# Optimization experiments

Hardware: AMD Instinct MI355X
Metric: run time of the kernel (lower is better)

## Reference

```python
import jax, jax.numpy as jnp
import numpy as np

# Graph sampling geometry (2-layer neighbor sampling, fanouts 16 and 10)
N0 = 1_048_576   # layer-0 src nodes (full frontier, features supplied)
N1 = 65_536      # layer-0 dst nodes == layer-1 src nodes
N2 = 4_096       # layer-1 dst nodes (seeds)
DEG0, DEG1 = 16, 10
E0, E1 = N1 * DEG0, N2 * DEG1
D_IN, D_H, D_OUT = 128, 256, 47


def _init_linear(key, out_f, in_f):
    s = 1.0 / np.sqrt(in_f)
    return jax.random.uniform(key, (out_f, in_f), jnp.float32, -s, s)


def setup_inputs() -> dict:
    key = jax.random.key(0)
    ks = jax.random.split(key, 10)
    x = jax.random.normal(ks[0], (N0, D_IN), dtype=jnp.float32)
    # CSC: indptr over dst nodes (uniform degree), indices = src node ids
    indptr0 = jnp.arange(N1 + 1, dtype=jnp.int32) * DEG0
    indices0 = jax.random.randint(ks[1], (E0,), 0, N0, dtype=jnp.int32)
    indptr1 = jnp.arange(N2 + 1, dtype=jnp.int32) * DEG1
    indices1 = jax.random.randint(ks[2], (E1,), 0, N1, dtype=jnp.int32)
    return {
        "x": x,
        "indices0": indices0, "indptr0": indptr0,
        "indices1": indices1, "indptr1": indptr1,
        "Wl0": _init_linear(ks[3], D_H, D_IN), "bl0": jnp.zeros((D_H,), jnp.float32),
        "Wr0": _init_linear(ks[4], D_H, D_IN),
        "Wl1": _init_linear(ks[5], D_H, D_H), "bl1": jnp.zeros((D_H,), jnp.float32),
        "Wr1": _init_linear(ks[6], D_H, D_H),
        "Wo": _init_linear(ks[7], D_OUT, D_H), "bo": jnp.zeros((D_OUT,), jnp.float32),
    }


def expand_indptr(indptr, num_edges):
    # gb.expand_indptr: edge e -> dst j with indptr[j] <= e < indptr[j+1]
    e = jnp.arange(num_edges, dtype=indptr.dtype)
    return jnp.searchsorted(indptr, e, side="right") - 1


def sage_conv(h, src, dst, dst_size, Wl, bl, Wr):
    # PyG SAGEConv (mean aggr): lin_l(mean_{neighbors}) + lin_r(x_dst)
    msg = h[src]                                                    # [E, d]
    summed = jax.ops.segment_sum(msg, dst, num_segments=dst_size)  # [dst, d]
    cnt = jax.ops.segment_sum(jnp.ones_like(dst, dtype=h.dtype), dst,
                              num_segments=dst_size)
    mean = summed / jnp.maximum(cnt, 1.0)[:, None]
    return mean @ Wl.T + bl + h[:dst_size] @ Wr.T


def reference(x, indices0, indptr0, indices1, indptr1,
              Wl0, bl0, Wr0, Wl1, bl1, Wr1, Wo, bo):
    # layer 0
    dst0 = expand_indptr(indptr0, E0)
    h = sage_conv(x, indices0, dst0, N1, Wl0, bl0, Wr0)
    h = jax.nn.gelu(h, approximate=False)  # dropout p=0.0 -> identity
    # layer 1
    dst1 = expand_indptr(indptr1, E1)
    h = sage_conv(h, indices1, dst1, N2, Wl1, bl1, Wr1)
    h = jax.nn.gelu(h, approximate=False)
    # final projection
    return h @ Wo.T + bo
```

## Files before the change

### kernel.cpp

```cpp
#include <hip/hip_runtime.h>
#include <math.h>

#define N0 1048576
#define N1 65536
#define N2 4096
#define DEG0 16
#define DEG1 10
#define D_IN 128
#define D_H 256
#define D_OUT 47

typedef unsigned int uint32;
typedef __attribute__((ext_vector_type(8))) short bf16x8;
typedef __attribute__((ext_vector_type(4))) float f32x4;

__device__ __forceinline__ unsigned short f2b(float x) {
    uint32 u = __float_as_uint(x);
    return (unsigned short)((u + 0x7fffu + ((u >> 16) & 1u)) >> 16);
}
__device__ __forceinline__ float b2f(unsigned short h) {
    return __uint_as_float(((uint32)h) << 16);
}
__device__ __forceinline__ float gelu_exact(float x) {
    return 0.5f * x * (1.0f + erff(x * 0.70710678118654752f));
}
__device__ __forceinline__ void split4(const float4 v, ushort4& h, ushort4& l) {
    h.x = f2b(v.x); l.x = f2b(v.x - b2f(h.x));
    h.y = f2b(v.y); l.y = f2b(v.y - b2f(h.y));
    h.z = f2b(v.z); l.z = f2b(v.z - b2f(h.z));
    h.w = f2b(v.w); l.w = f2b(v.w - b2f(h.w));
}

__global__ __launch_bounds__(256) void prep_all(
    const float4* __restrict__ Wl0, const float4* __restrict__ Wr0,
    const float4* __restrict__ Wl1, const float4* __restrict__ Wr1,
    const float4* __restrict__ Wo,  const float* __restrict__ bo,
    ushort4* __restrict__ wl0h, ushort4* __restrict__ wl0l,
    ushort4* __restrict__ wr0h, ushort4* __restrict__ wr0l,
    ushort4* __restrict__ wl1h, ushort4* __restrict__ wl1l,
    ushort4* __restrict__ wr1h, ushort4* __restrict__ wr1l,
    ushort4* __restrict__ woh,  ushort4* __restrict__ wol,
    float* __restrict__ bo_pad)
{
    int i = blockIdx.x * 256 + threadIdx.x;
    if (i >= 53248) return;
    const float4* src; ushort4 *dh, *dl; int rel;
    if (i < 8192)       { rel = i;         src = Wl0 + rel; dh = wl0h + rel; dl = wl0l + rel; }
    else if (i < 16384) { rel = i - 8192;  src = Wr0 + rel; dh = wr0h + rel; dl = wr0l + rel; }
    else if (i < 32768) { rel = i - 16384; src = Wl1 + rel; dh = wl1h + rel; dl = wl1l + rel; }
    else if (i < 49152) { rel = i - 32768; src = Wr1 + rel; dh = wr1h + rel; dl = wr1l + rel; }
    else {
        rel = i - 49152;
        float4 v = make_float4(0.f, 0.f, 0.f, 0.f);
        if (((rel * 4) >> 8) < D_OUT) v = Wo[rel];
        ushort4 h, l; split4(v, h, l);
        woh[rel] = h; wol[rel] = l;
        if (rel < 64) bo_pad[rel] = (rel < D_OUT) ? bo[rel] : 0.f;
        return;
    }
    float4 v = *src;
    ushort4 h, l; split4(v, h, l);
    *dh = h; *dl = l;
}

template <int DEG, int F4>
__global__ __launch_bounds__(256) void agg_split_bf16(
    const ushort4* __restrict__ fh, const ushort4* __restrict__ fl,
    const int* __restrict__ idx,
    ushort4* __restrict__ oh, ushort4* __restrict__ ol, int ndst)
{
    const int lane  = threadIdx.x % F4;
    const int local = threadIdx.x / F4;
    const int j = blockIdx.x * (256 / F4) + local;
    if (j >= ndst) return;

    const int* ip = idx + (long)j * DEG;
    int srcs[DEG];
#pragma unroll
    for (int e = 0; e < DEG; ++e) srcs[e] = ip[e];

    float4 acc = make_float4(0.f, 0.f, 0.f, 0.f);
#pragma unroll
    for (int e = 0; e < DEG; ++e) {
        long o = (long)srcs[e] * F4 + lane;
        ushort4 h = fh[o], l = fl[o];
        acc.x += b2f(h.x) + b2f(l.x);
        acc.y += b2f(h.y) + b2f(l.y);
        acc.z += b2f(h.z) + b2f(l.z);
        acc.w += b2f(h.w) + b2f(l.w);
    }
    const float r = 1.0f / (float)DEG;
    acc.x *= r; acc.y *= r; acc.z *= r; acc.w *= r;
    ushort4 h, l; split4(acc, h, l);
    oh[(long)j * F4 + lane] = h;
    ol[(long)j * F4 + lane] = l;
}

template <int K1, int K2, bool GELU, bool SPLIT_OUT>
__global__ __launch_bounds__(256) void gemm_mfma(
    const unsigned short* __restrict__ A1h, const unsigned short* __restrict__ A1l,
    const unsigned short* __restrict__ A2h, const unsigned short* __restrict__ A2l,
    const unsigned short* __restrict__ B1h, const unsigned short* __restrict__ B1l,
    const unsigned short* __restrict__ B2h, const unsigned short* __restrict__ B2l,
    const float* __restrict__ bias,
    float* __restrict__ Cf, unsigned short* __restrict__ Ch, unsigned short* __restrict__ Cl,
    int ldc, int ncols)
{
    constexpr int BK = 32, LDK = 40;
    __shared__ unsigned short sA[2][128][LDK];
    __shared__ unsigned short sB[2][64][LDK];

    const int tid  = threadIdx.x;
    const int bm   = blockIdx.x, bn = blockIdx.y;
    const int w    = tid >> 6;
    const int lane = tid & 63;
    const int quad = lane >> 4;
    const int l16  = lane & 15;

    f32x4 acc[2][4];
#pragma unroll
    for (int mt = 0; mt < 2; ++mt)
#pragma unroll
        for (int nt = 0; nt < 4; ++nt) acc[mt][nt] = (f32x4)0.f;

    constexpr int KT = (K1 + K2) / BK;
    for (int kt = 0; kt < KT; ++kt) {
        const int k0 = kt * BK;
        const unsigned short *Ah, *Al, *Bh, *Bl;
        int ka, koff;
        if (k0 < K1) { Ah = A1h; Al = A1l; Bh = B1h; Bl = B1l; ka = K1; koff = k0; }
        else         { Ah = A2h; Al = A2l; Bh = B2h; Bl = B2l; ka = (K2 ? K2 : 1); koff = k0 - K1; }

#pragma unroll
        for (int rep = 0; rep < 2; ++rep) {
            int task = tid + rep * 256;
            int row = task >> 2, seg = task & 3;
            size_t g = (size_t)(bm * 128 + row) * ka + koff + seg * 8;
            *(uint4*)&sA[0][row][seg * 8] = *(const uint4*)(Ah + g);
            *(uint4*)&sA[1][row][seg * 8] = *(const uint4*)(Al + g);
        }
        {
            int row = tid >> 2, seg = tid & 3;
            size_t g = (size_t)(bn * 64 + row) * ka + koff + seg * 8;
            *(uint4*)&sB[0][row][seg * 8] = *(const uint4*)(Bh + g);
            *(uint4*)&sB[1][row][seg * 8] = *(const uint4*)(Bl + g);
        }
        __syncthreads();

        bf16x8 Afh[2], Afl[2], Bfh[4], Bfl[4];
#pragma unroll
        for (int mt = 0; mt < 2; ++mt) {
            int r = w * 32 + mt * 16 + l16;
            Afh[mt] = *(const bf16x8*)&sA[0][r][quad * 8];
            Afl[mt] = *(const bf16x8*)&sA[1][r][quad * 8];
        }
#pragma unroll
        for (int nt = 0; nt < 4; ++nt) {
            int r = nt * 16 + l16;
            Bfh[nt] = *(const bf16x8*)&sB[0][r][quad * 8];
            Bfl[nt] = *(const bf16x8*)&sB[1][r][quad * 8];
        }
#pragma unroll
        for (int mt = 0; mt < 2; ++mt)
#pragma unroll
            for (int nt = 0; nt < 4; ++nt) {
                acc[mt][nt] = __builtin_amdgcn_mfma_f32_16x16x32_bf16(
                    Afl[mt], Bfh[nt], acc[mt][nt], 0, 0, 0);
                acc[mt][nt] = __builtin_amdgcn_mfma_f32_16x16x32_bf16(
                    Afh[mt], Bfl[nt], acc[mt][nt], 0, 0, 0);
                acc[mt][nt] = __builtin_amdgcn_mfma_f32_16x16x32_bf16(
                    Afh[mt], Bfh[nt], acc[mt][nt], 0, 0, 0);
            }
        __syncthreads();
    }

#pragma unroll
    for (int mt = 0; mt < 2; ++mt) {
        const int row0 = bm * 128 + w * 32 + mt * 16 + quad * 4;
#pragma unroll
        for (int nt = 0; nt < 4; ++nt) {
            const int col = bn * 64 + nt * 16 + l16;
            const float bb = bias[col];
#pragma unroll
            for (int r = 0; r < 4; ++r) {
                float v = acc[mt][nt][r] + bb;
                if (GELU) v = gelu_exact(v);
                if (SPLIT_OUT) {
                    unsigned short h = f2b(v);
                    Ch[(size_t)(row0 + r) * ldc + col] = h;
                    Cl[(size_t)(row0 + r) * ldc + col] = f2b(v - b2f(h));
                } else {
                    if (col < ncols) Cf[(size_t)(row0 + r) * ldc + col] = v;
                }
            }
        }
    }
}

__global__ __launch_bounds__(256) void l0_fused(
    const float4* __restrict__ x4, const int* __restrict__ idx0,
    const unsigned short* __restrict__ B1h, const unsigned short* __restrict__ B1l,
    const unsigned short* __restrict__ B2h, const unsigned short* __restrict__ B2l,
    const float* __restrict__ bias,
    unsigned short* __restrict__ Ch, unsigned short* __restrict__ Cl)
{
    constexpr int LDK = 40;
    __shared__ int sIdx[128 * DEG0];
    __shared__ unsigned short sA[2][128][LDK];
    __shared__ unsigned short sB[2][64][LDK];

    const int tid  = threadIdx.x;
    const int bm   = blockIdx.x;
    const int w    = tid >> 6;
    const int l64  = tid & 63;
    const int quad = l64 >> 4;
    const int l16  = l64 & 15;
    const int lane = tid & 31;
    const int grp  = tid >> 5;

    {
        const int4* s = (const int4*)(idx0 + (size_t)bm * (128 * DEG0));
        int4* d = (int4*)sIdx;
        d[tid]       = s[tid];
        d[tid + 256] = s[tid + 256];
    }
    __syncthreads();

    ushort4 ah[16], al[16];
#pragma unroll
    for (int i = 0; i < 16; ++i) {
        const int rb = (grp * 16 + i) * DEG0;
        float4 a = make_float4(0.f, 0.f, 0.f, 0.f);
#pragma unroll
        for (int e = 0; e < DEG0; ++e) {
            const float4 v = x4[(size_t)sIdx[rb + e] * (D_IN / 4) + lane];
            a.x += v.x; a.y += v.y; a.z += v.z; a.w += v.w;
        }
        const float r = 1.0f / (float)DEG0;
        a.x *= r; a.y *= r; a.z *= r; a.w *= r;
        split4(a, ah[i], al[i]);
    }

    const int arow  = tid >> 1;
    const int ahalf = tid & 1;

    for (int bn = 0; bn < 4; ++bn) {
        f32x4 acc[2][4];
#pragma unroll
        for (int mt = 0; mt < 2; ++mt)
#pragma unroll
            for (int nt = 0; nt < 4; ++nt) acc[mt][nt] = (f32x4)0.f;

#pragma unroll
        for (int kt = 0; kt < 8; ++kt) {
            const int k0 = kt * 32;
            if (kt < 4) {
                if ((lane >> 3) == kt) {
                    const int c = (lane & 7) * 4;
#pragma unroll
                    for (int i = 0; i < 16; ++i) {
                        const int rr = grp * 16 + i;
                        *(ushort4*)&sA[0][rr][c] = ah[i];
                        *(ushort4*)&sA[1][rr][c] = al[i];
                    }
                }
            } else {
                const float4* sx = x4 + (size_t)(bm * 128 + arow) * (D_IN / 4)
                                      + (kt - 4) * 8 + ahalf * 4;
#pragma unroll
                for (int q = 0; q < 4; ++q) {
                    ushort4 h, l;
                    split4(sx[q], h, l);
                    const int c = ahalf * 16 + q * 4;
                    *(ushort4*)&sA[0][arow][c] = h;
                    *(ushort4*)&sA[1][arow][c] = l;
                }
            }
            {
                const int row = tid >> 2, seg = tid & 3;
                const unsigned short *Bh, *Bl; int koff;
                if (k0 < D_IN) { Bh = B1h; Bl = B1l; koff = k0; }
                else           { Bh = B2h; Bl = B2l; koff = k0 - D_IN; }
                const size_t g = (size_t)(bn * 64 + row) * D_IN + koff + seg * 8;
                *(uint4*)&sB[0][row][seg * 8] = *(const uint4*)(Bh + g);
                *(uint4*)&sB[1][row][seg * 8] = *(const uint4*)(Bl + g);
            }
            __syncthreads();

            bf16x8 Afh[2], Afl[2];
#pragma unroll
            for (int mt = 0; mt < 2; ++mt) {
                const int r = w * 32 + mt * 16 + l16;
                Afh[mt] = *(const bf16x8*)&sA[0][r][quad * 8];
                Afl[mt] = *(const bf16x8*)&sA[1][r][quad * 8];
            }
#pragma unroll
            for (int nt = 0; nt < 4; ++nt) {
                const int r = nt * 16 + l16;
                const bf16x8 Bfh = *(const bf16x8*)&sB[0][r][quad * 8];
                const bf16x8 Bfl = *(const bf16x8*)&sB[1][r][quad * 8];
#pragma unroll
                for (int mt = 0; mt < 2; ++mt) {
                    acc[mt][nt] = __builtin_amdgcn_mfma_f32_16x16x32_bf16(
                        Afl[mt], Bfh, acc[mt][nt], 0, 0, 0);
                    acc[mt][nt] = __builtin_amdgcn_mfma_f32_16x16x32_bf16(
                        Afh[mt], Bfl, acc[mt][nt], 0, 0, 0);
                    acc[mt][nt] = __builtin_amdgcn_mfma_f32_16x16x32_bf16(
                        Afh[mt], Bfh, acc[mt][nt], 0, 0, 0);
                }
            }
            __syncthreads();
        }

#pragma unroll
        for (int mt = 0; mt < 2; ++mt) {
            const int row0 = bm * 128 + w * 32 + mt * 16 + quad * 4;
#pragma unroll
            for (int nt = 0; nt < 4; ++nt) {
                const int col = bn * 64 + nt * 16 + l16;
                const float bb = bias[col];
#pragma unroll
                for (int r = 0; r < 4; ++r) {
                    float v = gelu_exact(acc[mt][nt][r] + bb);
                    const unsigned short h = f2b(v);
                    Ch[(size_t)(row0 + r) * D_H + col] = h;
                    Cl[(size_t)(row0 + r) * D_H + col] = f2b(v - b2f(h));
                }
            }
        }
    }
}

extern "C" void kernel_launch(void* const* d_in, const int* in_sizes, int n_in,
                              void* d_out, int out_size, void* d_ws, size_t ws_size,
                              hipStream_t stream)
{
    const float* x        = (const float*)d_in[0];
    const int*   indices0 = (const int*)d_in[1];
    const int*   indices1 = (const int*)d_in[3];
    const float* Wl0 = (const float*)d_in[5];
    const float* bl0 = (const float*)d_in[6];
    const float* Wr0 = (const float*)d_in[7];
    const float* Wl1 = (const float*)d_in[8];
    const float* bl1 = (const float*)d_in[9];
    const float* Wr1 = (const float*)d_in[10];
    const float* Wo  = (const float*)d_in[11];
    const float* bo  = (const float*)d_in[12];
    float* out = (float*)d_out;

    unsigned short* p = (unsigned short*)d_ws;
    unsigned short* h0h  = p; p += (size_t)N1 * D_H;
    unsigned short* h0l  = p; p += (size_t)N1 * D_H;
    unsigned short* m1h  = p; p += (size_t)N2 * D_H;
    unsigned short* m1l  = p; p += (size_t)N2 * D_H;
    unsigned short* h1h  = p; p += (size_t)N2 * D_H;
    unsigned short* h1l  = p; p += (size_t)N2 * D_H;
    unsigned short* wl0h = p; p += 256 * 128;
    unsigned short* wl0l = p; p += 256 * 128;
    unsigned short* wr0h = p; p += 256 * 128;
    unsigned short* wr0l = p; p += 256 * 128;
    unsigned short* wl1h = p; p += 256 * 256;
    unsigned short* wl1l = p; p += 256 * 256;
    unsigned short* wr1h = p; p += 256 * 256;
    unsigned short* wr1l = p; p += 256 * 256;
    unsigned short* woh  = p; p += 64 * 256;
    unsigned short* wol  = p; p += 64 * 256;
    float* bo_pad = (float*)p;

    prep_all<<<208, 256, 0, stream>>>(
        (const float4*)Wl0, (const float4*)Wr0, (const float4*)Wl1, (const float4*)Wr1,
        (const float4*)Wo, bo,
        (ushort4*)wl0h, (ushort4*)wl0l, (ushort4*)wr0h, (ushort4*)wr0l,
        (ushort4*)wl1h, (ushort4*)wl1l, (ushort4*)wr1h, (ushort4*)wr1l,
        (ushort4*)woh, (ushort4*)wol, bo_pad);

    l0_fused<<<N1 / 128, 256, 0, stream>>>(
        (const float4*)x, indices0, wl0h, wl0l, wr0h, wr0l, bl0, h0h, h0l);

    agg_split_bf16<DEG1, D_H / 4><<<N2 / (256 / (D_H / 4)), 256, 0, stream>>>(
        (const ushort4*)h0h, (const ushort4*)h0l, indices1, (ushort4*)m1h, (ushort4*)m1l, N2);

    gemm_mfma<D_H, D_H, true, true><<<dim3(N2 / 128, D_H / 64), 256, 0, stream>>>(
        m1h, m1l, h0h, h0l, wl1h, wl1l, wr1h, wr1l, bl1,
        nullptr, h1h, h1l, D_H, D_H);

    gemm_mfma<D_H, 0, false, false><<<dim3(N2 / 128, 1), 256, 0, stream>>>(
        h1h, h1l, h1h, h1l, woh, wol, woh, wol, bo_pad,
        out, nullptr, nullptr, D_OUT, D_OUT);
}
```

Baseline: 772.4 us.

## Shrink layer-0 fused block to 64 rows with 128-wide N tiles

The fused layer-0 gather+GEMM kernel now processes 64 destination rows per block instead of 128, doubling the grid to 1024 blocks. Each wave handles one 16-row M tile against eight 16-column N tiles, with two 128-column N passes instead of four 64-column passes. Fewer gather accumulators per thread and the launch-bounds hint of 4 blocks per CU are meant to raise occupancy and hide the random gather latency. In exchange, the B weight tile is reloaded by twice as many blocks and per-block LDS for B doubles.

```diff
diff --git a/kernel.cpp b/kernel.cpp
--- a/kernel.cpp
+++ b/kernel.cpp
@@ -197,17 +197,17 @@
     }
 }
 
-__global__ __launch_bounds__(256) void l0_fused(
+__global__ __launch_bounds__(256, 4) void l0_fused(
     const float4* __restrict__ x4, const int* __restrict__ idx0,
     const unsigned short* __restrict__ B1h, const unsigned short* __restrict__ B1l,
     const unsigned short* __restrict__ B2h, const unsigned short* __restrict__ B2l,
     const float* __restrict__ bias,
     unsigned short* __restrict__ Ch, unsigned short* __restrict__ Cl)
 {
-    constexpr int LDK = 40;
-    __shared__ int sIdx[128 * DEG0];
-    __shared__ unsigned short sA[2][128][LDK];
-    __shared__ unsigned short sB[2][64][LDK];
+    constexpr int BM = 64, LDK = 40;
+    __shared__ int sIdx[BM * DEG0];
+    __shared__ unsigned short sA[2][BM][LDK];
+    __shared__ unsigned short sB[2][128][LDK];
 
     const int tid  = threadIdx.x;
     const int bm   = blockIdx.x;
@@ -219,17 +219,15 @@
     const int grp  = tid >> 5;
 
     {
-        const int4* s = (const int4*)(idx0 + (size_t)bm * (128 * DEG0));
-        int4* d = (int4*)sIdx;
-        d[tid]       = s[tid];
-        d[tid + 256] = s[tid + 256];
+        const int4* s = (const int4*)(idx0 + (size_t)bm * (BM * DEG0));
+        ((int4*)sIdx)[tid] = s[tid];
     }
     __syncthreads();
 
-    ushort4 ah[16], al[16];
-#pragma unroll
-    for (int i = 0; i < 16; ++i) {
-        const int rb = (grp * 16 + i) * DEG0;
+    ushort4 ah[8], al[8];
+#pragma unroll
+    for (int i = 0; i < 8; ++i) {
+        const int rb = (grp * 8 + i) * DEG0;
         float4 a = make_float4(0.f, 0.f, 0.f, 0.f);
 #pragma unroll
         for (int e = 0; e < DEG0; ++e) {
@@ -241,15 +239,10 @@
         split4(a, ah[i], al[i]);
     }
 
-    const int arow  = tid >> 1;
-    const int ahalf = tid & 1;
-
-    for (int bn = 0; bn < 4; ++bn) {
-        f32x4 acc[2][4];
-#pragma unroll
-        for (int mt = 0; mt < 2; ++mt)
-#pragma unroll
-            for (int nt = 0; nt < 4; ++nt) acc[mt][nt] = (f32x4)0.f;
+    for (int bn = 0; bn < 2; ++bn) {
+        f32x4 acc[8];
+#pragma unroll
+        for (int nt = 0; nt < 8; ++nt) acc[nt] = (f32x4)0.f;
 
 #pragma unroll
         for (int kt = 0; kt < 8; ++kt) {
@@ -258,74 +251,67 @@
                 if ((lane >> 3) == kt) {
                     const int c = (lane & 7) * 4;
 #pragma unroll
-                    for (int i = 0; i < 16; ++i) {
-                        const int rr = grp * 16 + i;
+                    for (int i = 0; i < 8; ++i) {
+                        const int rr = grp * 8 + i;
                         *(ushort4*)&sA[0][rr][c] = ah[i];
                         *(ushort4*)&sA[1][rr][c] = al[i];
                     }
                 }
             } else {
-                const float4* sx = x4 + (size_t)(bm * 128 + arow) * (D_IN / 4)
-                                      + (kt - 4) * 8 + ahalf * 4;
-#pragma unroll
-                for (int q = 0; q < 4; ++q) {
+                const int arow = tid >> 2, aseg = tid & 3;
+                const float4* sx = x4 + (size_t)(bm * BM + arow) * (D_IN / 4)
+                                      + (kt - 4) * 8 + aseg * 2;
+#pragma unroll
+                for (int q = 0; q < 2; ++q) {
                     ushort4 h, l;
                     split4(sx[q], h, l);
-                    const int c = ahalf * 16 + q * 4;
+                    const int c = aseg * 8 + q * 4;
                     *(ushort4*)&sA[0][arow][c] = h;
                     *(ushort4*)&sA[1][arow][c] = l;
                 }
             }
-            {
-                const int row = tid >> 2, seg = tid & 3;
+#pragma unroll
+            for (int rep = 0; rep < 2; ++rep) {
+                const int task = tid + rep * 256;
+                const int row = task >> 2, seg = task & 3;
                 const unsigned short *Bh, *Bl; int koff;
                 if (k0 < D_IN) { Bh = B1h; Bl = B1l; koff = k0; }
                 else           { Bh = B2h; Bl = B2l; koff = k0 - D_IN; }
-                const size_t g = (size_t)(bn * 64 + row) * D_IN + koff + seg * 8;
+                const size_t g = (size_t)(bn * 128 + row) * D_IN + koff + seg * 8;
                 *(uint4*)&sB[0][row][seg * 8] = *(const uint4*)(Bh + g);
                 *(uint4*)&sB[1][row][seg * 8] = *(const uint4*)(Bl + g);
             }
             __syncthreads();
 
-            bf16x8 Afh[2], Afl[2];
-#pragma unroll
-            for (int mt = 0; mt < 2; ++mt) {
-                const int r = w * 32 + mt * 16 + l16;
-                Afh[mt] = *(const bf16x8*)&sA[0][r][quad * 8];
-                Afl[mt] = *(const bf16x8*)&sA[1][r][quad * 8];
-            }
-#pragma unroll
-            for (int nt = 0; nt < 4; ++nt) {
-                const int r = nt * 16 + l16;
-                const bf16x8 Bfh = *(const bf16x8*)&sB[0][r][quad * 8];
-                const bf16x8 Bfl = *(const bf16x8*)&sB[1][r][quad * 8];
-#pragma unroll
-                for (int mt = 0; mt < 2; ++mt) {
-                    acc[mt][nt] = __builtin_amdgcn_mfma_f32_16x16x32_bf16(
-                        Afl[mt], Bfh, acc[mt][nt], 0, 0, 0);
-                    acc[mt][nt] = __builtin_amdgcn_mfma_f32_16x16x32_bf16(
-                        Afh[mt], Bfl, acc[mt][nt], 0, 0, 0);
-                    acc[mt][nt] = __builtin_amdgcn_mfma_f32_16x16x32_bf16(
-                        Afh[mt], Bfh, acc[mt][nt], 0, 0, 0);
-                }
+            const int r = w * 16 + l16;
+            const bf16x8 Afh = *(const bf16x8*)&sA[0][r][quad * 8];
+            const bf16x8 Afl = *(const bf16x8*)&sA[1][r][quad * 8];
+#pragma unroll
+            for (int nt = 0; nt < 8; ++nt) {
+                const int rb2 = nt * 16 + l16;
+                const bf16x8 Bfh = *(const bf16x8*)&sB[0][rb2][quad * 8];
+                const bf16x8 Bfl = *(const bf16x8*)&sB[1][rb2][quad * 8];
+                acc[nt] = __builtin_amdgcn_mfma_f32_16x16x32_bf16(
+                    Afl, Bfh, acc[nt], 0, 0, 0);
+                acc[nt] = __builtin_amdgcn_mfma_f32_16x16x32_bf16(
+                    Afh, Bfl, acc[nt], 0, 0, 0);
+                acc[nt] = __builtin_amdgcn_mfma_f32_16x16x32_bf16(
+                    Afh, Bfh, acc[nt], 0, 0, 0);
             }
             __syncthreads();
         }
 
-#pragma unroll
-        for (int mt = 0; mt < 2; ++mt) {
-            const int row0 = bm * 128 + w * 32 + mt * 16 + quad * 4;
-#pragma unroll
-            for (int nt = 0; nt < 4; ++nt) {
-                const int col = bn * 64 + nt * 16 + l16;
-                const float bb = bias[col];
-#pragma unroll
-                for (int r = 0; r < 4; ++r) {
-                    float v = gelu_exact(acc[mt][nt][r] + bb);
-                    const unsigned short h = f2b(v);
-                    Ch[(size_t)(row0 + r) * D_H + col] = h;
-                    Cl[(size_t)(row0 + r) * D_H + col] = f2b(v - b2f(h));
-                }
+        const int row0 = bm * BM + w * 16 + quad * 4;
+#pragma unroll
+        for (int nt = 0; nt < 8; ++nt) {
+            const int col = bn * 128 + nt * 16 + l16;
+            const float bb = bias[col];
+#pragma unroll
+            for (int r2 = 0; r2 < 4; ++r2) {
+                float v = gelu_exact(acc[nt][r2] + bb);
+                const unsigned short h = f2b(v);
+                Ch[(size_t)(row0 + r2) * D_H + col] = h;
+                Cl[(size_t)(row0 + r2) * D_H + col] = f2b(v - b2f(h));
             }
         }
     }
@@ -374,7 +360,7 @@
         (ushort4*)wl1h, (ushort4*)wl1l, (ushort4*)wr1h, (ushort4*)wr1l,
         (ushort4*)woh, (ushort4*)wol, bo_pad);
 
-    l0_fused<<<N1 / 128, 256, 0, stream>>>(
+    l0_fused<<<N1 / 64, 256, 0, stream>>>(
         (const float4*)x, indices0, wl0h, wl0l, wr0h, wr0l, bl0, h0h, h0l);
 
     agg_split_bf16<DEG1, D_H / 4><<<N2 / (256 / (D_H / 4)), 256, 0, stream>>>(
```

New measurement: 781.2 us. Within noise of the previous version (+1.1%).
